# Kernel tuning notes

Hardware: AMD Instinct MI355X
Metric: run time of the kernel (lower is better)

Reference implementation:

```python
import jax, jax.numpy as jnp
import numpy as np

INPUT_DIM = 20000
UNITS = 4096
NNZ = 800000
BATCH = 1024


def setup_inputs() -> dict:
    key = jax.random.key(0)
    k1, k2, k3, k4 = jax.random.split(key, 4)
    x = jax.random.normal(k1, (BATCH, INPUT_DIM), dtype=jnp.float32)
    kernel_vector = jax.random.normal(k2, (NNZ,), dtype=jnp.float32) * 0.05
    bias = jnp.zeros((UNITS,), dtype=jnp.float32)
    rows = jax.random.randint(k3, (NNZ,), 0, INPUT_DIM, dtype=jnp.int32)
    cols = jax.random.randint(k4, (NNZ,), 0, UNITS, dtype=jnp.int32)
    nonzero_ind = jnp.stack([rows, cols], axis=1)  # [NNZ, 2]
    return {"x": x, "kernel_vector": kernel_vector, "bias": bias, "nonzero_ind": nonzero_ind}


def reference(x, kernel_vector, bias, nonzero_ind):
    # scatter_nd: build dense (input_dim, units) kernel; duplicates accumulate (matches tf.scatter_nd)
    input_dim = x.shape[1]
    units = bias.shape[0]
    dense_kernel = jnp.zeros((input_dim, units), dtype=kernel_vector.dtype)
    dense_kernel = dense_kernel.at[nonzero_ind[:, 0], nonzero_ind[:, 1]].add(kernel_vector)
    out = jnp.matmul(x, dense_kernel) + bias  # [B, units]
    return jnp.tanh(out)
```

## Files before the change

### kernel.cpp

```cpp
#include <hip/hip_runtime.h>
#include <hip/hip_fp16.h>

#define BATCH      1024
#define INPUT_DIM  20000
#define UNITS      4096
#define NNZ        800000
#define BAND_ROW   10000
#define CAP        192
#define NSLOT      (UNITS * 2)

#define WS_XT    0
#define WS_CNT   40960000
#define WS_OFFS  (WS_CNT + 32768)
#define WS_VALS  (WS_OFFS + NSLOT * CAP * 4)

__global__ __launch_bounds__(256) void transpose_in_kernel(
    const float* __restrict__ x, unsigned int* __restrict__ xTu,
    int* __restrict__ cnt) {
    int t = threadIdx.x;
    int flat = blockIdx.y * gridDim.x + blockIdx.x;
    int gid = flat * 256 + t;
    if (gid < NSLOT) cnt[gid] = 0;

    __shared__ float tile[64][33];
    int d0 = blockIdx.x * 32;
    int b0 = blockIdx.y * 64;
    int dl = t & 31;
    int bl0 = t >> 5;
#pragma unroll
    for (int i = 0; i < 64; i += 8)
        tile[bl0 + i][dl] = x[(size_t)(b0 + bl0 + i) * INPUT_DIM + d0 + dl];
    __syncthreads();
    int bp = t & 31;
    int dl0 = t >> 5;
#pragma unroll
    for (int i = 0; i < 32; i += 8) {
        int d = dl0 + i;
        unsigned short lo = __half_as_ushort(__float2half(tile[2 * bp][d]));
        unsigned short hi = __half_as_ushort(__float2half(tile[2 * bp + 1][d]));
        xTu[(size_t)(d0 + d) * (BATCH / 2) + (b0 >> 1) + bp] =
            (unsigned int)lo | ((unsigned int)hi << 16);
    }
}

__global__ void scatter_kernel(const int* __restrict__ ind, const float* __restrict__ vals_in,
                               int* __restrict__ cnt, unsigned int* __restrict__ offs,
                               float* __restrict__ vals) {
    int i = blockIdx.x * blockDim.x + threadIdx.x;
    if (i < NNZ) {
        int r = ind[2 * i];
        int c = ind[2 * i + 1];
        int band = (r >= BAND_ROW) ? 1 : 0;
        int slot = (c << 1) + band;
        int pos = atomicAdd(&cnt[slot], 1);
        if (pos < CAP) {
            offs[slot * CAP + pos] = (unsigned int)r << 10;
            vals[slot * CAP + pos] = vals_in[i];
        }
    }
}

__global__ __launch_bounds__(512, 8) void spmm_kernel(
    const unsigned int* __restrict__ offs, const float* __restrict__ vals,
    const int* __restrict__ cnt, const unsigned short* __restrict__ xT,
    const float* __restrict__ bias, float* __restrict__ out) {
    __shared__ float tile[128][33];
    int bid = blockIdx.x;
    int kLow = bid & 7;
    int cg = bid >> 3;
    int tid = threadIdx.x;
    int lane = tid & 63;
    int w = __builtin_amdgcn_readfirstlane(tid >> 6);
    int colbase = (cg << 5) + (w << 2);
    unsigned int laneoff = (unsigned int)(kLow << 7) + (unsigned int)(lane << 1);

    float acc[4][2] = {{0.f, 0.f}, {0.f, 0.f}, {0.f, 0.f}, {0.f, 0.f}};
#pragma unroll
    for (int bd = 0; bd < 2; ++bd) {
#pragma unroll
        for (int c = 0; c < 4; ++c) {
            int slot = ((colbase + c) << 1) + bd;
            int n = cnt[slot];
            if (n > CAP) n = CAP;
            const unsigned int* ob = offs + slot * CAP;
            const float* vb = vals + slot * CAP;
            float a0 = acc[c][0], a1 = acc[c][1];
            int j = 0;
            for (; j + 4 <= n; j += 4) {
                uint4 o4 = *(const uint4*)(ob + j);
                float4 v4 = *(const float4*)(vb + j);
                __half2 h0 = *(const __half2*)(xT + (o4.x + laneoff));
                __half2 h1 = *(const __half2*)(xT + (o4.y + laneoff));
                __half2 h2 = *(const __half2*)(xT + (o4.z + laneoff));
                __half2 h3 = *(const __half2*)(xT + (o4.w + laneoff));
                a0 = fmaf(__half2float(__low2half(h0)),  v4.x, a0);
                a1 = fmaf(__half2float(__high2half(h0)), v4.x, a1);
                a0 = fmaf(__half2float(__low2half(h1)),  v4.y, a0);
                a1 = fmaf(__half2float(__high2half(h1)), v4.y, a1);
                a0 = fmaf(__half2float(__low2half(h2)),  v4.z, a0);
                a1 = fmaf(__half2float(__high2half(h2)), v4.z, a1);
                a0 = fmaf(__half2float(__low2half(h3)),  v4.w, a0);
                a1 = fmaf(__half2float(__high2half(h3)), v4.w, a1);
            }
            for (; j < n; ++j) {
                __half2 h = *(const __half2*)(xT + (ob[j] + laneoff));
                float v = vb[j];
                a0 = fmaf(__half2float(__low2half(h)),  v, a0);
                a1 = fmaf(__half2float(__high2half(h)), v, a1);
            }
            acc[c][0] = a0; acc[c][1] = a1;
        }
    }

    int r0 = lane << 1;
#pragma unroll
    for (int c = 0; c < 4; ++c) {
        float bc = bias[colbase + c];
        tile[r0][(w << 2) + c]     = tanhf(acc[c][0] + bc);
        tile[r0 + 1][(w << 2) + c] = tanhf(acc[c][1] + bc);
    }
    __syncthreads();
    int bl = tid >> 2;
    int c0 = (tid & 3) << 3;
    float4 u0 = make_float4(tile[bl][c0],     tile[bl][c0 + 1],
                            tile[bl][c0 + 2], tile[bl][c0 + 3]);
    float4 u1 = make_float4(tile[bl][c0 + 4], tile[bl][c0 + 5],
                            tile[bl][c0 + 6], tile[bl][c0 + 7]);
    size_t obase = (size_t)((kLow << 7) + bl) * UNITS + (cg << 5) + c0;
    *(float4*)(out + obase)     = u0;
    *(float4*)(out + obase + 4) = u1;
}

extern "C" void kernel_launch(void* const* d_in, const int* in_sizes, int n_in,
                              void* d_out, int out_size, void* d_ws, size_t ws_size,
                              hipStream_t stream) {
    const float* x    = (const float*)d_in[0];
    const float* vals = (const float*)d_in[1];
    const float* bias = (const float*)d_in[2];
    const int*   ind  = (const int*)d_in[3];
    float* out = (float*)d_out;

    char* ws = (char*)d_ws;
    unsigned short* xT  = (unsigned short*)(ws + WS_XT);
    int*          cnt   = (int*)(ws + WS_CNT);
    unsigned int* offsA = (unsigned int*)(ws + WS_OFFS);
    float*        valsA = (float*)(ws + WS_VALS);

    transpose_in_kernel<<<dim3(INPUT_DIM / 32, BATCH / 64), 256, 0, stream>>>(
        x, (unsigned int*)xT, cnt);
    scatter_kernel<<<NNZ / 256, 256, 0, stream>>>(ind, vals, cnt, offsA, valsA);
    spmm_kernel<<<1024, 512, 0, stream>>>(offsA, valsA, cnt, xT, bias, out);
}
```

Before: 307.7 us.

## Restructure SpMM to wide 16-byte gathers with interleaved index/value pairs

Packs row offsets and values into interleaved uint2 pairs and zero-fills the whole pair buffer so padded entries contribute nothing. The SpMM kernel now has each lane load 16 bytes (8 batch halves), with four lane groups splitting the nonzeros of a column and reducing via shuffles. Each block covers 16 columns instead of 32 and the grid doubles to 2048 blocks. The transpose kernel also switches to float4 reads and uint2 writes. The trade-off is extra zeroing traffic, wasted work on padded entries, and shuffle reductions in exchange for wider, fewer gather instructions.

```diff
diff --git a/kernel.cpp b/kernel.cpp
--- a/kernel.cpp
+++ b/kernel.cpp
@@ -9,126 +9,126 @@
 #define CAP        192
 #define NSLOT      (UNITS * 2)
 
-#define WS_XT    0
-#define WS_CNT   40960000
-#define WS_OFFS  (WS_CNT + 32768)
-#define WS_VALS  (WS_OFFS + NSLOT * CAP * 4)
+#define WS_XT     0
+#define WS_CNT    40960000
+#define WS_PAIRS  (WS_CNT + 32768)
+#define ZERO_INTS (NSLOT + NSLOT * CAP * 2)
 
 __global__ __launch_bounds__(256) void transpose_in_kernel(
-    const float* __restrict__ x, unsigned int* __restrict__ xTu,
-    int* __restrict__ cnt) {
+    const float4* __restrict__ x4, unsigned int* __restrict__ xTu,
+    uint2* __restrict__ zbase) {
     int t = threadIdx.x;
-    int flat = blockIdx.y * gridDim.x + blockIdx.x;
-    int gid = flat * 256 + t;
-    if (gid < NSLOT) cnt[gid] = 0;
+    unsigned int gid = (blockIdx.y * gridDim.x + blockIdx.x) * 256 + t;
+    if (gid < ZERO_INTS / 2) zbase[gid] = make_uint2(0u, 0u);
 
     __shared__ float tile[64][33];
     int d0 = blockIdx.x * 32;
     int b0 = blockIdx.y * 64;
-    int dl = t & 31;
-    int bl0 = t >> 5;
+
+    int fx = t & 7, rr = t >> 3;
 #pragma unroll
-    for (int i = 0; i < 64; i += 8)
-        tile[bl0 + i][dl] = x[(size_t)(b0 + bl0 + i) * INPUT_DIM + d0 + dl];
+    for (int p = 0; p < 2; p++) {
+        int b = rr + p * 32;
+        float4 v = x4[(size_t)(b0 + b) * (INPUT_DIM / 4) + (d0 >> 2) + fx];
+        tile[b][fx * 4 + 0] = v.x; tile[b][fx * 4 + 1] = v.y;
+        tile[b][fx * 4 + 2] = v.z; tile[b][fx * 4 + 3] = v.w;
+    }
     __syncthreads();
-    int bp = t & 31;
-    int dl0 = t >> 5;
+    int bq = t & 15, dd = t >> 4;
 #pragma unroll
-    for (int i = 0; i < 32; i += 8) {
-        int d = dl0 + i;
-        unsigned short lo = __half_as_ushort(__float2half(tile[2 * bp][d]));
-        unsigned short hi = __half_as_ushort(__float2half(tile[2 * bp + 1][d]));
-        xTu[(size_t)(d0 + d) * (BATCH / 2) + (b0 >> 1) + bp] =
-            (unsigned int)lo | ((unsigned int)hi << 16);
+    for (int p = 0; p < 2; p++) {
+        int d = dd + p * 16;
+        unsigned short h0 = __half_as_ushort(__float2half(tile[bq * 4 + 0][d]));
+        unsigned short h1 = __half_as_ushort(__float2half(tile[bq * 4 + 1][d]));
+        unsigned short h2 = __half_as_ushort(__float2half(tile[bq * 4 + 2][d]));
+        unsigned short h3 = __half_as_ushort(__float2half(tile[bq * 4 + 3][d]));
+        uint2 u = make_uint2((unsigned)h0 | ((unsigned)h1 << 16),
+                             (unsigned)h2 | ((unsigned)h3 << 16));
+        *(uint2*)(xTu + (size_t)(d0 + d) * (BATCH / 2) + (b0 >> 1) + bq * 2) = u;
     }
 }
 
-__global__ void scatter_kernel(const int* __restrict__ ind, const float* __restrict__ vals_in,
-                               int* __restrict__ cnt, unsigned int* __restrict__ offs,
-                               float* __restrict__ vals) {
+__global__ void scatter_kernel(const int2* __restrict__ ind2, const float* __restrict__ vals_in,
+                               int* __restrict__ cnt, uint2* __restrict__ pairs) {
     int i = blockIdx.x * blockDim.x + threadIdx.x;
     if (i < NNZ) {
-        int r = ind[2 * i];
-        int c = ind[2 * i + 1];
-        int band = (r >= BAND_ROW) ? 1 : 0;
-        int slot = (c << 1) + band;
+        int2 rc = ind2[i];
+        int band = (rc.x >= BAND_ROW) ? 1 : 0;
+        int slot = (rc.y << 1) + band;
         int pos = atomicAdd(&cnt[slot], 1);
-        if (pos < CAP) {
-            offs[slot * CAP + pos] = (unsigned int)r << 10;
-            vals[slot * CAP + pos] = vals_in[i];
-        }
+        if (pos < CAP)
+            pairs[slot * CAP + pos] =
+                make_uint2((unsigned)rc.x << 11, __float_as_uint(vals_in[i]));
+    }
+}
+
+__device__ __forceinline__ void accum8(uint4 q, float v, float* a) {
+    const __half2* h = (const __half2*)&q;
+#pragma unroll
+    for (int i = 0; i < 4; i++) {
+        a[2 * i]     = fmaf(__half2float(__low2half(h[i])),  v, a[2 * i]);
+        a[2 * i + 1] = fmaf(__half2float(__high2half(h[i])), v, a[2 * i + 1]);
     }
 }
 
 __global__ __launch_bounds__(512, 8) void spmm_kernel(
-    const unsigned int* __restrict__ offs, const float* __restrict__ vals,
-    const int* __restrict__ cnt, const unsigned short* __restrict__ xT,
-    const float* __restrict__ bias, float* __restrict__ out) {
-    __shared__ float tile[128][33];
+    const uint2* __restrict__ pairs, const int* __restrict__ cnt,
+    const char* __restrict__ xTb, const float* __restrict__ bias,
+    float* __restrict__ out) {
+    __shared__ float tile[128][17];
     int bid = blockIdx.x;
     int kLow = bid & 7;
     int cg = bid >> 3;
     int tid = threadIdx.x;
     int lane = tid & 63;
-    int w = __builtin_amdgcn_readfirstlane(tid >> 6);
-    int colbase = (cg << 5) + (w << 2);
-    unsigned int laneoff = (unsigned int)(kLow << 7) + (unsigned int)(lane << 1);
+    int w = tid >> 6;
+    int g = lane >> 4;
+    int s = lane & 15;
+    unsigned int laneterm = (unsigned)(kLow << 8) + (unsigned)(s << 4);
+    int colbase = (cg << 4) + (w << 1);
 
-    float acc[4][2] = {{0.f, 0.f}, {0.f, 0.f}, {0.f, 0.f}, {0.f, 0.f}};
+    float a[2][8] = {{0.f,0.f,0.f,0.f,0.f,0.f,0.f,0.f},
+                     {0.f,0.f,0.f,0.f,0.f,0.f,0.f,0.f}};
 #pragma unroll
     for (int bd = 0; bd < 2; ++bd) {
 #pragma unroll
-        for (int c = 0; c < 4; ++c) {
+        for (int c = 0; c < 2; ++c) {
             int slot = ((colbase + c) << 1) + bd;
             int n = cnt[slot];
             if (n > CAP) n = CAP;
-            const unsigned int* ob = offs + slot * CAP;
-            const float* vb = vals + slot * CAP;
-            float a0 = acc[c][0], a1 = acc[c][1];
-            int j = 0;
-            for (; j + 4 <= n; j += 4) {
-                uint4 o4 = *(const uint4*)(ob + j);
-                float4 v4 = *(const float4*)(vb + j);
-                __half2 h0 = *(const __half2*)(xT + (o4.x + laneoff));
-                __half2 h1 = *(const __half2*)(xT + (o4.y + laneoff));
-                __half2 h2 = *(const __half2*)(xT + (o4.z + laneoff));
-                __half2 h3 = *(const __half2*)(xT + (o4.w + laneoff));
-                a0 = fmaf(__half2float(__low2half(h0)),  v4.x, a0);
-                a1 = fmaf(__half2float(__high2half(h0)), v4.x, a1);
-                a0 = fmaf(__half2float(__low2half(h1)),  v4.y, a0);
-                a1 = fmaf(__half2float(__high2half(h1)), v4.y, a1);
-                a0 = fmaf(__half2float(__low2half(h2)),  v4.z, a0);
-                a1 = fmaf(__half2float(__high2half(h2)), v4.z, a1);
-                a0 = fmaf(__half2float(__low2half(h3)),  v4.w, a0);
-                a1 = fmaf(__half2float(__high2half(h3)), v4.w, a1);
+            int npad = (n + 7) & ~7;
+            const uint2* pb = pairs + slot * CAP + g;
+            float* ac = a[c];
+            for (int j = 0; j < npad; j += 8) {
+                uint2 e0 = pb[j];
+                uint2 e1 = pb[j + 4];
+                uint4 q0 = *(const uint4*)(xTb + (e0.x + laneterm));
+                uint4 q1 = *(const uint4*)(xTb + (e1.x + laneterm));
+                accum8(q0, __uint_as_float(e0.y), ac);
+                accum8(q1, __uint_as_float(e1.y), ac);
             }
-            for (; j < n; ++j) {
-                __half2 h = *(const __half2*)(xT + (ob[j] + laneoff));
-                float v = vb[j];
-                a0 = fmaf(__half2float(__low2half(h)),  v, a0);
-                a1 = fmaf(__half2float(__high2half(h)), v, a1);
-            }
-            acc[c][0] = a0; acc[c][1] = a1;
         }
     }
 
-    int r0 = lane << 1;
 #pragma unroll
-    for (int c = 0; c < 4; ++c) {
+    for (int c = 0; c < 2; ++c) {
         float bc = bias[colbase + c];
-        tile[r0][(w << 2) + c]     = tanhf(acc[c][0] + bc);
-        tile[r0 + 1][(w << 2) + c] = tanhf(acc[c][1] + bc);
+#pragma unroll
+        for (int i = 0; i < 8; i++) {
+            float v = a[c][i];
+            v += __shfl_xor(v, 16, 64);
+            v += __shfl_xor(v, 32, 64);
+            if (g == 0)
+                tile[(s << 3) + i][(w << 1) + c] = tanhf(v + bc);
+        }
     }
     __syncthreads();
+
     int bl = tid >> 2;
-    int c0 = (tid & 3) << 3;
-    float4 u0 = make_float4(tile[bl][c0],     tile[bl][c0 + 1],
+    int c0 = (tid & 3) << 2;
+    float4 vv = make_float4(tile[bl][c0], tile[bl][c0 + 1],
                             tile[bl][c0 + 2], tile[bl][c0 + 3]);
-    float4 u1 = make_float4(tile[bl][c0 + 4], tile[bl][c0 + 5],
-                            tile[bl][c0 + 6], tile[bl][c0 + 7]);
-    size_t obase = (size_t)((kLow << 7) + bl) * UNITS + (cg << 5) + c0;
-    *(float4*)(out + obase)     = u0;
-    *(float4*)(out + obase + 4) = u1;
+    *(float4*)(out + (size_t)((kLow << 7) + bl) * UNITS + (cg << 4) + c0) = vv;
 }
 
 extern "C" void kernel_launch(void* const* d_in, const int* in_sizes, int n_in,
@@ -141,13 +141,12 @@
     float* out = (float*)d_out;
 
     char* ws = (char*)d_ws;
-    unsigned short* xT  = (unsigned short*)(ws + WS_XT);
-    int*          cnt   = (int*)(ws + WS_CNT);
-    unsigned int* offsA = (unsigned int*)(ws + WS_OFFS);
-    float*        valsA = (float*)(ws + WS_VALS);
+    char*  xT    = ws + WS_XT;
+    int*   cnt   = (int*)(ws + WS_CNT);
+    uint2* pairs = (uint2*)(ws + WS_PAIRS);
 
     transpose_in_kernel<<<dim3(INPUT_DIM / 32, BATCH / 64), 256, 0, stream>>>(
-        x, (unsigned int*)xT, cnt);
-    scatter_kernel<<<NNZ / 256, 256, 0, stream>>>(ind, vals, cnt, offsA, valsA);
-    spmm_kernel<<<1024, 512, 0, stream>>>(offsA, valsA, cnt, xT, bias, out);
+        (const float4*)x, (unsigned int*)xT, (uint2*)(ws + WS_CNT));
+    scatter_kernel<<<NNZ / 256, 256, 0, stream>>>((const int2*)ind, vals, cnt, pairs);
+    spmm_kernel<<<2048, 512, 0, stream>>>(pairs, cnt, xT, bias, out);
 }
```

Result: faster. 291.0 us (-5.4%).
